# Kernel tuning notes

Hardware: AMD Instinct MI355X
Metric: run time of the kernel (lower is better)

Reference implementation:

```python
import jax, jax.numpy as jnp
import numpy as np

N_NODES = 50000
N_EDGES = 800000
IN_CH = 64
HID = 64
N_LAYERS = 4


def setup_inputs() -> dict:
    key = jax.random.key(0)
    ks = jax.random.split(key, 10)
    x = jax.random.normal(ks[0], (N_NODES, IN_CH), dtype=jnp.float32)
    edge_index = jax.random.randint(ks[1], (2, N_EDGES), 0, N_NODES, dtype=jnp.int32)
    # SAGEConv params per layer: lin_l (applied to aggregated neighbors, with bias)
    # and lin_r (applied to root node). All layers are 64->64 so stack to [L, in, out].
    s = 1.0 / np.sqrt(IN_CH)
    Wl = jax.random.uniform(ks[2], (N_LAYERS, IN_CH, HID), jnp.float32, -s, s)
    Wr = jax.random.uniform(ks[3], (N_LAYERS, IN_CH, HID), jnp.float32, -s, s)
    b = jax.random.uniform(ks[4], (N_LAYERS, HID), jnp.float32, -s, s)
    alpha = jnp.full((N_LAYERS, HID), 0.25, dtype=jnp.float32)  # PReLU init
    return {"x": x, "edge_index": edge_index, "Wl": Wl, "Wr": Wr, "b": b, "alpha": alpha}


def _sage_layer(x, src, dst, deg_inv, Wl, Wr, b):
    # mean aggregation of source-node features at destination nodes
    agg = jax.ops.segment_sum(x[src], dst, num_segments=N_NODES)  # [N, d]
    agg = agg * deg_inv[:, None]
    return agg @ Wl + x @ Wr + b


def _prelu(x, a):
    return jnp.where(x >= 0, x, a * x)


def reference(x, edge_index, Wl, Wr, b, alpha):
    src, dst = edge_index[0], edge_index[1]
    deg = jax.ops.segment_sum(jnp.ones((N_EDGES,), jnp.float32), dst, num_segments=N_NODES)
    deg_inv = 1.0 / jnp.maximum(deg, 1.0)
    for i in range(N_LAYERS):
        x = _sage_layer(x, src, dst, deg_inv, Wl[i], Wr[i], b[i])
        x = _prelu(x, alpha[i])
    return x
```

## Files before the change

kernel.cpp:

```cpp
#include <hip/hip_runtime.h>

#define NN 50000
#define NE 800000
#define C 64
#define NL 4
#define SCAN_NB 196

typedef __attribute__((ext_vector_type(8))) short bf16x8;
typedef __attribute__((ext_vector_type(4))) float f32x4;

__device__ __forceinline__ unsigned short f2bf(float f) {
    unsigned u = __float_as_uint(f);
    u += 0x7fffu + ((u >> 16) & 1u);
    return (unsigned short)(u >> 16);
}
__device__ __forceinline__ float4 bf4_to_f4(uint2 p) {
    float4 r;
    r.x = __uint_as_float(p.x << 16);
    r.y = __uint_as_float(p.x & 0xffff0000u);
    r.z = __uint_as_float(p.y << 16);
    r.w = __uint_as_float(p.y & 0xffff0000u);
    return r;
}

__global__ void init_kernel(int4* __restrict__ p) {
    int i = blockIdx.x * blockDim.x + threadIdx.x;
    if (i < (NN + 16) / 4) p[i] = make_int4(0, 0, 0, 0);
}

__global__ void hist_rank_kernel(const int* __restrict__ dst, int* __restrict__ deg_cnt,
                                 int* __restrict__ rank) {
    int e = blockIdx.x * blockDim.x + threadIdx.x;
    if (e < NE) rank[e] = atomicAdd(&deg_cnt[dst[e]], 1);
}

__global__ __launch_bounds__(256) void scan1_kernel(const int* __restrict__ deg_cnt,
                                                    int* __restrict__ row_start,
                                                    int* __restrict__ bsums) {
    __shared__ int sdata[256];
    int tid = threadIdx.x;
    int i = blockIdx.x * 256 + tid;
    int v = (i < NN) ? deg_cnt[i] : 0;
    sdata[tid] = v;
    __syncthreads();
    for (int off = 1; off < 256; off <<= 1) {
        int t = (tid >= off) ? sdata[tid - off] : 0;
        __syncthreads();
        sdata[tid] += t;
        __syncthreads();
    }
    int incl = sdata[tid];
    if (i < NN) row_start[i] = incl - v;
    if (tid == 255) bsums[blockIdx.x] = incl;
}

__global__ __launch_bounds__(256) void scan23_kernel(int* __restrict__ row_start,
                                                     const int* __restrict__ bsums,
                                                     const int* __restrict__ deg_cnt,
                                                     float* __restrict__ deg_inv) {
    __shared__ int sdata[256];
    int tid = threadIdx.x;
    int v = (tid < SCAN_NB) ? bsums[tid] : 0;
    sdata[tid] = v;
    __syncthreads();
    for (int off = 1; off < 256; off <<= 1) {
        int t = (tid >= off) ? sdata[tid - off] : 0;
        __syncthreads();
        sdata[tid] += t;
        __syncthreads();
    }
    int b = blockIdx.x;
    int offset = (b == 0) ? 0 : sdata[b - 1];
    int i = b * 256 + tid;
    if (i < NN) {
        row_start[i] += offset;
        deg_inv[i] = 1.0f / fmaxf((float)deg_cnt[i], 1.0f);
    }
}

__global__ void fill_kernel(const int* __restrict__ src, const int* __restrict__ dst,
                            const int* __restrict__ rank, const int* __restrict__ row_start,
                            int* __restrict__ csr_src) {
    int t = blockIdx.x * blockDim.x + threadIdx.x;
    int e0 = t * 4;
    if (e0 + 3 < NE) {
        int4 d4 = ((const int4*)dst)[t];
        int4 r4 = ((const int4*)rank)[t];
        int4 s4 = ((const int4*)src)[t];
        csr_src[row_start[d4.x] + r4.x] = s4.x;
        csr_src[row_start[d4.y] + r4.y] = s4.y;
        csr_src[row_start[d4.z] + r4.z] = s4.z;
        csr_src[row_start[d4.w] + r4.w] = s4.w;
    } else if (e0 < NE) {
        for (int e = e0; e < NE; e++)
            csr_src[row_start[dst[e]] + rank[e]] = src[e];
    }
}

__global__ __launch_bounds__(512) void transform_mfma_kernel(
    const float* __restrict__ xin,
    const float* __restrict__ Wl, const float* __restrict__ Wr,
    const float* __restrict__ bias,
    unsigned short* __restrict__ y, float* __restrict__ z)
{
    __shared__ unsigned short xs[64][72];
    __shared__ unsigned short wlT[64][72];
    __shared__ unsigned short wrT[64][72];
    __shared__ unsigned short ys[64][64];
    __shared__ float zs[64][64];
    __shared__ float bs[C];

    int tid = threadIdx.x;
    int node0 = blockIdx.x * 64;

    for (int i = tid; i < C * C; i += 512) {
        int k = i >> 6, c = i & 63;
        wlT[c][k] = f2bf(Wl[i]);
        wrT[c][k] = f2bf(Wr[i]);
    }
    if (tid < C) bs[tid] = bias[tid];
    for (int i = tid; i < 64 * 16; i += 512) {
        int nl = i >> 4, c4 = i & 15;
        int n = node0 + nl;
        int nc = n < NN ? n : NN - 1;
        float4 v = ((const float4*)xin)[(size_t)nc * 16 + c4];
        xs[nl][c4 * 4 + 0] = f2bf(v.x);
        xs[nl][c4 * 4 + 1] = f2bf(v.y);
        xs[nl][c4 * 4 + 2] = f2bf(v.z);
        xs[nl][c4 * 4 + 3] = f2bf(v.w);
    }
    __syncthreads();

    int w = tid >> 6;
    int l = tid & 63;
    int mt = w >> 1;
    int half = w & 1;
    int r16 = l & 15;
    int kg = l >> 4;

    bf16x8 a0 = *(const bf16x8*)&xs[mt * 16 + r16][kg * 8];
    bf16x8 a1 = *(const bf16x8*)&xs[mt * 16 + r16][32 + kg * 8];

    f32x4 acc[4];
    #pragma unroll
    for (int nt = 0; nt < 4; nt++) {
        float bv = half ? bs[nt * 16 + r16] : 0.f;
        acc[nt] = (f32x4){bv, bv, bv, bv};
    }
    #pragma unroll
    for (int nt = 0; nt < 4; nt++) {
        const unsigned short* col = half ? &wrT[nt * 16 + r16][0] : &wlT[nt * 16 + r16][0];
        bf16x8 b0 = *(const bf16x8*)&col[kg * 8];
        bf16x8 b1 = *(const bf16x8*)&col[32 + kg * 8];
        acc[nt] = __builtin_amdgcn_mfma_f32_16x16x32_bf16(a0, b0, acc[nt], 0, 0, 0);
        acc[nt] = __builtin_amdgcn_mfma_f32_16x16x32_bf16(a1, b1, acc[nt], 0, 0, 0);
    }
    #pragma unroll
    for (int nt = 0; nt < 4; nt++) {
        #pragma unroll
        for (int j = 0; j < 4; j++) {
            int r = mt * 16 + kg * 4 + j;
            int c = nt * 16 + r16;
            if (half) zs[r][c] = acc[nt][j];
            else      ys[r][c] = f2bf(acc[nt][j]);
        }
    }
    __syncthreads();

    for (int i = tid; i < 64 * 16; i += 512) {
        int r = i >> 4, g = i & 15;
        int n = node0 + r;
        if (n < NN) {
            ((ushort4*)&y[(size_t)n * C])[g] = ((const ushort4*)&ys[r][0])[g];
            ((float4*)&z[(size_t)n * C])[g] = ((const float4*)&zs[r][0])[g];
        }
    }
}

__device__ __forceinline__ float4 gather_row(const uint2* __restrict__ yb,
                                             const int* __restrict__ cp, int d, int ql) {
    float4 acc = make_float4(0.f, 0.f, 0.f, 0.f);
    for (int t = 0; t < d; t += 8) {
        int lim = d - 1 - t;
        int j1 = min(1, lim), j2 = min(2, lim), j3 = min(3, lim);
        int j4 = min(4, lim), j5 = min(5, lim), j6 = min(6, lim), j7 = min(7, lim);
        float m1 = lim >= 1 ? 1.f : 0.f, m2 = lim >= 2 ? 1.f : 0.f;
        float m3 = lim >= 3 ? 1.f : 0.f, m4 = lim >= 4 ? 1.f : 0.f;
        float m5 = lim >= 5 ? 1.f : 0.f, m6 = lim >= 6 ? 1.f : 0.f;
        float m7 = lim >= 7 ? 1.f : 0.f;
        int s0 = cp[t];
        int s1 = cp[t + j1];
        int s2 = cp[t + j2];
        int s3 = cp[t + j3];
        int s4 = cp[t + j4];
        int s5 = cp[t + j5];
        int s6 = cp[t + j6];
        int s7 = cp[t + j7];
        uint2 p0 = yb[(size_t)s0 * 16 + ql];
        uint2 p1 = yb[(size_t)s1 * 16 + ql];
        uint2 p2 = yb[(size_t)s2 * 16 + ql];
        uint2 p3 = yb[(size_t)s3 * 16 + ql];
        uint2 p4 = yb[(size_t)s4 * 16 + ql];
        uint2 p5 = yb[(size_t)s5 * 16 + ql];
        uint2 p6 = yb[(size_t)s6 * 16 + ql];
        uint2 p7 = yb[(size_t)s7 * 16 + ql];
        float4 v0 = bf4_to_f4(p0);
        float4 v1 = bf4_to_f4(p1);
        float4 v2 = bf4_to_f4(p2);
        float4 v3 = bf4_to_f4(p3);
        float4 v4 = bf4_to_f4(p4);
        float4 v5 = bf4_to_f4(p5);
        float4 v6 = bf4_to_f4(p6);
        float4 v7 = bf4_to_f4(p7);
        acc.x += v0.x;      acc.y += v0.y;      acc.z += v0.z;      acc.w += v0.w;
        acc.x += v1.x * m1; acc.y += v1.y * m1; acc.z += v1.z * m1; acc.w += v1.w * m1;
        acc.x += v2.x * m2; acc.y += v2.y * m2; acc.z += v2.z * m2; acc.w += v2.w * m2;
        acc.x += v3.x * m3; acc.y += v3.y * m3; acc.z += v3.z * m3; acc.w += v3.w * m3;
        acc.x += v4.x * m4; acc.y += v4.y * m4; acc.z += v4.z * m4; acc.w += v4.w * m4;
        acc.x += v5.x * m5; acc.y += v5.y * m5; acc.z += v5.z * m5; acc.w += v5.w * m5;
        acc.x += v6.x * m6; acc.y += v6.y * m6; acc.z += v6.z * m6; acc.w += v6.w * m6;
        acc.x += v7.x * m7; acc.y += v7.y * m7; acc.z += v7.z * m7; acc.w += v7.w * m7;
    }
    return acc;
}

__global__ __launch_bounds__(512) void fused_gt_kernel(
    const uint2* __restrict__ yb, const float4* __restrict__ z4,
    const int* __restrict__ row_start, const int* __restrict__ deg_cnt,
    const float* __restrict__ deg_inv, const float* __restrict__ alpha,
    const int* __restrict__ csr_src,
    const float* __restrict__ Wl2, const float* __restrict__ Wr2,
    const float* __restrict__ bias2,
    unsigned short* __restrict__ yout, float* __restrict__ zout)
{
    __shared__ unsigned short wlT[64][72];
    __shared__ unsigned short wrT[64][72];
    __shared__ unsigned short xsb[32][72];
    __shared__ unsigned short ys[32][64];
    __shared__ float zs[32][64];
    __shared__ float bs2[C];

    int tid = threadIdx.x;
    for (int i = tid; i < C * C; i += 512) {
        int k = i >> 6, c = i & 63;
        wlT[c][k] = f2bf(Wl2[i]);
        wrT[c][k] = f2bf(Wr2[i]);
    }
    if (tid < C) bs2[tid] = bias2[tid];

    int nl = tid >> 4;
    int ql = tid & 15;
    int n = blockIdx.x * 32 + nl;

    float4 o = make_float4(0.f, 0.f, 0.f, 0.f);
    if (n < NN) {
        int rs = row_start[n];
        int d = deg_cnt[n];
        float4 acc = gather_row(yb, csr_src + rs, d, ql);
        float di = deg_inv[n];
        float4 zz = z4[(size_t)n * 16 + ql];
        float4 a4 = ((const float4*)alpha)[ql];
        o.x = di * acc.x + zz.x;
        o.y = di * acc.y + zz.y;
        o.z = di * acc.z + zz.z;
        o.w = di * acc.w + zz.w;
        o.x = o.x >= 0.f ? o.x : a4.x * o.x;
        o.y = o.y >= 0.f ? o.y : a4.y * o.y;
        o.z = o.z >= 0.f ? o.z : a4.z * o.z;
        o.w = o.w >= 0.f ? o.w : a4.w * o.w;
    }
    {
        ushort4 p = make_ushort4(f2bf(o.x), f2bf(o.y), f2bf(o.z), f2bf(o.w));
        *(ushort4*)&xsb[nl][ql * 4] = p;
    }
    __syncthreads();

    int w = tid >> 6;
    int l = tid & 63;
    int mt = w & 1;
    int half = (w >> 1) & 1;
    int ntg = w >> 2;
    int r16 = l & 15;
    int kg = l >> 4;

    bf16x8 a0 = *(const bf16x8*)&xsb[mt * 16 + r16][kg * 8];
    bf16x8 a1 = *(const bf16x8*)&xsb[mt * 16 + r16][32 + kg * 8];

    #pragma unroll
    for (int q = 0; q < 2; q++) {
        int nt = ntg * 2 + q;
        const unsigned short* col = half ? &wrT[nt * 16 + r16][0] : &wlT[nt * 16 + r16][0];
        bf16x8 b0 = *(const bf16x8*)&col[kg * 8];
        bf16x8 b1 = *(const bf16x8*)&col[32 + kg * 8];
        float bv = half ? bs2[nt * 16 + r16] : 0.f;
        f32x4 acc = (f32x4){bv, bv, bv, bv};
        acc = __builtin_amdgcn_mfma_f32_16x16x32_bf16(a0, b0, acc, 0, 0, 0);
        acc = __builtin_amdgcn_mfma_f32_16x16x32_bf16(a1, b1, acc, 0, 0, 0);
        #pragma unroll
        for (int j = 0; j < 4; j++) {
            int r = mt * 16 + kg * 4 + j;
            int c = nt * 16 + r16;
            if (half) zs[r][c] = acc[j];
            else      ys[r][c] = f2bf(acc[j]);
        }
    }
    __syncthreads();

    {
        int r = tid >> 4, g = tid & 15;
        int n2 = blockIdx.x * 32 + r;
        if (n2 < NN) {
            ((ushort4*)&yout[(size_t)n2 * C])[g] = ((const ushort4*)&ys[r][0])[g];
            ((float4*)&zout[(size_t)n2 * C])[g] = ((const float4*)&zs[r][0])[g];
        }
    }
}

__global__ __launch_bounds__(256) void gather_kernel(
    const uint2* __restrict__ yb, const float4* __restrict__ z4,
    const int* __restrict__ row_start, const int* __restrict__ deg_cnt,
    const float* __restrict__ deg_inv, const float* __restrict__ alpha,
    const int* __restrict__ csr_src,
    float4* __restrict__ out4)
{
    int tid = threadIdx.x;
    int n = blockIdx.x * 16 + (tid >> 4);
    int ql = tid & 15;

    int rs = row_start[n];
    int d = deg_cnt[n];
    float4 acc = gather_row(yb, csr_src + rs, d, ql);

    float di = deg_inv[n];
    float4 zz = z4[(size_t)n * 16 + ql];
    float4 a4 = ((const float4*)alpha)[ql];
    float4 o;
    o.x = di * acc.x + zz.x;
    o.y = di * acc.y + zz.y;
    o.z = di * acc.z + zz.z;
    o.w = di * acc.w + zz.w;
    o.x = o.x >= 0.f ? o.x : a4.x * o.x;
    o.y = o.y >= 0.f ? o.y : a4.y * o.y;
    o.z = o.z >= 0.f ? o.z : a4.z * o.z;
    o.w = o.w >= 0.f ? o.w : a4.w * o.w;
    out4[(size_t)n * 16 + ql] = o;
}

extern "C" void kernel_launch(void* const* d_in, const int* in_sizes, int n_in,
                              void* d_out, int out_size, void* d_ws, size_t ws_size,
                              hipStream_t stream) {
    const float* x     = (const float*)d_in[0];
    const int*   ei    = (const int*)d_in[1];
    const float* Wl    = (const float*)d_in[2];
    const float* Wr    = (const float*)d_in[3];
    const float* b     = (const float*)d_in[4];
    const float* alpha = (const float*)d_in[5];
    float* out = (float*)d_out;

    const int* src = ei;
    const int* dst = ei + NE;

    char* wsp = (char*)d_ws;
    int*   deg_cnt   = (int*)wsp;                   wsp += (size_t)(NN + 16) * 4;
    float* deg_inv   = (float*)wsp;                 wsp += (size_t)NN * 4;
    int*   row_start = (int*)wsp;                   wsp += (size_t)NN * 4;
    int*   bsums     = (int*)wsp;                   wsp += 1024;
    int*   rankb     = (int*)wsp;                   wsp += (size_t)NE * 4;
    int*   csr_src   = (int*)wsp;                   wsp += (size_t)NE * 4;
    unsigned short* y0buf = (unsigned short*)wsp;   wsp += (size_t)NN * C * 2;
    unsigned short* y1buf = (unsigned short*)wsp;   wsp += (size_t)NN * C * 2;
    float* z0buf     = (float*)wsp;                 wsp += (size_t)NN * C * 4;
    float* z1buf     = (float*)wsp;

    init_kernel<<<49, 256, 0, stream>>>((int4*)deg_cnt);
    hist_rank_kernel<<<(NE + 255) / 256, 256, 0, stream>>>(dst, deg_cnt, rankb);
    scan1_kernel<<<SCAN_NB, 256, 0, stream>>>(deg_cnt, row_start, bsums);
    scan23_kernel<<<SCAN_NB, 256, 0, stream>>>(row_start, bsums, deg_cnt, deg_inv);
    fill_kernel<<<(NE / 4 + 255) / 256, 256, 0, stream>>>(src, dst, rankb, row_start, csr_src);

    transform_mfma_kernel<<<(NN + 63) / 64, 512, 0, stream>>>(x, Wl, Wr, b, y0buf, z0buf);

    const int fblocks = (NN + 31) / 32;
    unsigned short* ycur = y0buf; float* zcur = z0buf;
    unsigned short* ynxt = y1buf; float* znxt = z1buf;
    for (int l = 0; l < NL - 1; l++) {
        fused_gt_kernel<<<fblocks, 512, 0, stream>>>(
            (const uint2*)ycur, (const float4*)zcur,
            row_start, deg_cnt, deg_inv, alpha + (size_t)l * C, csr_src,
            Wl + (size_t)(l + 1) * C * C, Wr + (size_t)(l + 1) * C * C,
            b + (size_t)(l + 1) * C,
            ynxt, znxt);
        unsigned short* ty = ycur; float* tz = zcur;
        ycur = ynxt; zcur = znxt;
        ynxt = ty;   znxt = tz;
    }

    gather_kernel<<<NN / 16, 256, 0, stream>>>(
        (const uint2*)ycur, (const float4*)zcur, row_start, deg_cnt,
        deg_inv, alpha + (size_t)(NL - 1) * C, csr_src, (float4*)out);
}
```

Measured before the change: 172.2 us.

## Build CSR via two-level bucket sort with shared-memory atomics

Replaces the global-atomic histogram, rank and scatter CSR build with a two-level counting sort. Edges are first bucketed by dst>>8 using per-block shared-memory counters and a per-bucket prefix scan. Each 256-node bucket then computes degrees and fills CSR with local shared atomics. This avoids contended global atomics and random global scatter, at the cost of more kernel launches and an extra pass over an int2 sorted edge array. Within-node neighbor order becomes nondeterministic, but the sum is order-independent up to rounding.

```diff
diff --git a/kernel.cpp b/kernel.cpp
--- a/kernel.cpp
+++ b/kernel.cpp
@@ -5,6 +5,8 @@
 #define C 64
 #define NL 4
 #define SCAN_NB 196
+#define NBK 196
+#define HBLK 782
 
 typedef __attribute__((ext_vector_type(8))) short bf16x8;
 typedef __attribute__((ext_vector_type(4))) float f32x4;
@@ -23,24 +25,91 @@
     return r;
 }
 
-__global__ void init_kernel(int4* __restrict__ p) {
-    int i = blockIdx.x * blockDim.x + threadIdx.x;
-    if (i < (NN + 16) / 4) p[i] = make_int4(0, 0, 0, 0);
-}
-
-__global__ void hist_rank_kernel(const int* __restrict__ dst, int* __restrict__ deg_cnt,
-                                 int* __restrict__ rank) {
-    int e = blockIdx.x * blockDim.x + threadIdx.x;
-    if (e < NE) rank[e] = atomicAdd(&deg_cnt[dst[e]], 1);
-}
-
-__global__ __launch_bounds__(256) void scan1_kernel(const int* __restrict__ deg_cnt,
+__global__ __launch_bounds__(1024) void bucket_hist_kernel(const int* __restrict__ dst,
+                                                           int* __restrict__ blk_cnt,
+                                                           int* __restrict__ lrank) {
+    __shared__ int cnt[NBK];
+    int tid = threadIdx.x;
+    int blk = blockIdx.x;
+    if (tid < NBK) cnt[tid] = 0;
+    __syncthreads();
+    int e = blk * 1024 + tid;
+    if (e < NE) lrank[e] = atomicAdd(&cnt[dst[e] >> 8], 1);
+    __syncthreads();
+    if (tid < NBK) blk_cnt[tid * HBLK + blk] = cnt[tid];
+}
+
+__global__ __launch_bounds__(1024) void scanblk_kernel(int* __restrict__ blk_cnt,
+                                                       int* __restrict__ bucket_tot) {
+    __shared__ int sdata[1024];
+    int b = blockIdx.x;
+    int tid = threadIdx.x;
+    int v = (tid < HBLK) ? blk_cnt[b * HBLK + tid] : 0;
+    sdata[tid] = v;
+    __syncthreads();
+    for (int off = 1; off < 1024; off <<= 1) {
+        int t = (tid >= off) ? sdata[tid - off] : 0;
+        __syncthreads();
+        sdata[tid] += t;
+        __syncthreads();
+    }
+    if (tid < HBLK) blk_cnt[b * HBLK + tid] = sdata[tid] - v;
+    if (tid == HBLK - 1) bucket_tot[b] = sdata[tid];
+}
+
+__global__ __launch_bounds__(256) void scanbucket_kernel(const int* __restrict__ bucket_tot,
+                                                         int* __restrict__ bucket_start) {
+    __shared__ int sdata[256];
+    int tid = threadIdx.x;
+    int v = (tid < NBK) ? bucket_tot[tid] : 0;
+    sdata[tid] = v;
+    __syncthreads();
+    for (int off = 1; off < 256; off <<= 1) {
+        int t = (tid >= off) ? sdata[tid - off] : 0;
+        __syncthreads();
+        sdata[tid] += t;
+        __syncthreads();
+    }
+    if (tid < NBK) bucket_start[tid] = sdata[tid] - v;
+    if (tid == NBK - 1) bucket_start[NBK] = sdata[tid];
+}
+
+__global__ __launch_bounds__(1024) void bucket_scatter_kernel(
+    const int* __restrict__ src, const int* __restrict__ dst,
+    const int* __restrict__ lrank, const int* __restrict__ base2,
+    const int* __restrict__ bucket_start, int2* __restrict__ sorted) {
+    int blk = blockIdx.x;
+    int e = blk * 1024 + threadIdx.x;
+    if (e < NE) {
+        int d = dst[e];
+        int b = d >> 8;
+        int pos = bucket_start[b] + base2[b * HBLK + blk] + lrank[e];
+        sorted[pos] = make_int2(src[e], d);
+    }
+}
+
+__global__ __launch_bounds__(512) void bucket_deg_kernel(const int2* __restrict__ sorted,
+                                                         const int* __restrict__ bucket_start,
+                                                         int* __restrict__ deg) {
+    __shared__ int ldeg[256];
+    int b = blockIdx.x;
+    int tid = threadIdx.x;
+    if (tid < 256) ldeg[tid] = 0;
+    __syncthreads();
+    int lo = bucket_start[b], hi = bucket_start[b + 1];
+    for (int i = lo + tid; i < hi; i += 512)
+        atomicAdd(&ldeg[sorted[i].y & 255], 1);
+    __syncthreads();
+    if (tid < 256) deg[b * 256 + tid] = ldeg[tid];
+}
+
+__global__ __launch_bounds__(256) void scan1_kernel(const int* __restrict__ deg,
                                                     int* __restrict__ row_start,
                                                     int* __restrict__ bsums) {
     __shared__ int sdata[256];
     int tid = threadIdx.x;
     int i = blockIdx.x * 256 + tid;
-    int v = (i < NN) ? deg_cnt[i] : 0;
+    int v = (i < NN) ? deg[i] : 0;
     sdata[tid] = v;
     __syncthreads();
     for (int off = 1; off < 256; off <<= 1) {
@@ -56,7 +125,7 @@
 
 __global__ __launch_bounds__(256) void scan23_kernel(int* __restrict__ row_start,
                                                      const int* __restrict__ bsums,
-                                                     const int* __restrict__ deg_cnt,
+                                                     const int* __restrict__ deg,
                                                      float* __restrict__ deg_inv) {
     __shared__ int sdata[256];
     int tid = threadIdx.x;
@@ -74,26 +143,29 @@
     int i = b * 256 + tid;
     if (i < NN) {
         row_start[i] += offset;
-        deg_inv[i] = 1.0f / fmaxf((float)deg_cnt[i], 1.0f);
-    }
-}
-
-__global__ void fill_kernel(const int* __restrict__ src, const int* __restrict__ dst,
-                            const int* __restrict__ rank, const int* __restrict__ row_start,
-                            int* __restrict__ csr_src) {
-    int t = blockIdx.x * blockDim.x + threadIdx.x;
-    int e0 = t * 4;
-    if (e0 + 3 < NE) {
-        int4 d4 = ((const int4*)dst)[t];
-        int4 r4 = ((const int4*)rank)[t];
-        int4 s4 = ((const int4*)src)[t];
-        csr_src[row_start[d4.x] + r4.x] = s4.x;
-        csr_src[row_start[d4.y] + r4.y] = s4.y;
-        csr_src[row_start[d4.z] + r4.z] = s4.z;
-        csr_src[row_start[d4.w] + r4.w] = s4.w;
-    } else if (e0 < NE) {
-        for (int e = e0; e < NE; e++)
-            csr_src[row_start[dst[e]] + rank[e]] = src[e];
+        deg_inv[i] = 1.0f / fmaxf((float)deg[i], 1.0f);
+    }
+}
+
+__global__ __launch_bounds__(512) void bucket_fill_kernel(const int2* __restrict__ sorted,
+                                                          const int* __restrict__ bucket_start,
+                                                          const int* __restrict__ row_start,
+                                                          int* __restrict__ csr_src) {
+    __shared__ int rs[256];
+    __shared__ int lcnt[256];
+    int b = blockIdx.x;
+    int tid = threadIdx.x;
+    if (tid < 256) {
+        int n = b * 256 + tid;
+        rs[tid] = (n < NN) ? row_start[n] : 0;
+        lcnt[tid] = 0;
+    }
+    __syncthreads();
+    int lo = bucket_start[b], hi = bucket_start[b + 1];
+    for (int i = lo + tid; i < hi; i += 512) {
+        int2 p = sorted[i];
+        int r = atomicAdd(&lcnt[p.y & 255], 1);
+        csr_src[rs[p.y & 255] + r] = p.x;
     }
 }
 
@@ -226,7 +298,7 @@
 
 __global__ __launch_bounds__(512) void fused_gt_kernel(
     const uint2* __restrict__ yb, const float4* __restrict__ z4,
-    const int* __restrict__ row_start, const int* __restrict__ deg_cnt,
+    const int* __restrict__ row_start, const int* __restrict__ deg,
     const float* __restrict__ deg_inv, const float* __restrict__ alpha,
     const int* __restrict__ csr_src,
     const float* __restrict__ Wl2, const float* __restrict__ Wr2,
@@ -255,7 +327,7 @@
     float4 o = make_float4(0.f, 0.f, 0.f, 0.f);
     if (n < NN) {
         int rs = row_start[n];
-        int d = deg_cnt[n];
+        int d = deg[n];
         float4 acc = gather_row(yb, csr_src + rs, d, ql);
         float di = deg_inv[n];
         float4 zz = z4[(size_t)n * 16 + ql];
@@ -318,7 +390,7 @@
 
 __global__ __launch_bounds__(256) void gather_kernel(
     const uint2* __restrict__ yb, const float4* __restrict__ z4,
-    const int* __restrict__ row_start, const int* __restrict__ deg_cnt,
+    const int* __restrict__ row_start, const int* __restrict__ deg,
     const float* __restrict__ deg_inv, const float* __restrict__ alpha,
     const int* __restrict__ csr_src,
     float4* __restrict__ out4)
@@ -328,7 +400,7 @@
     int ql = tid & 15;
 
     int rs = row_start[n];
-    int d = deg_cnt[n];
+    int d = deg[n];
     float4 acc = gather_row(yb, csr_src + rs, d, ql);
 
     float di = deg_inv[n];
@@ -361,22 +433,30 @@
     const int* dst = ei + NE;
 
     char* wsp = (char*)d_ws;
-    int*   deg_cnt   = (int*)wsp;                   wsp += (size_t)(NN + 16) * 4;
-    float* deg_inv   = (float*)wsp;                 wsp += (size_t)NN * 4;
-    int*   row_start = (int*)wsp;                   wsp += (size_t)NN * 4;
-    int*   bsums     = (int*)wsp;                   wsp += 1024;
-    int*   rankb     = (int*)wsp;                   wsp += (size_t)NE * 4;
-    int*   csr_src   = (int*)wsp;                   wsp += (size_t)NE * 4;
+    int*  lrank        = (int*)wsp;                 wsp += (size_t)NE * 4;
+    int*  blk_cnt      = (int*)wsp;                 wsp += (size_t)NBK * HBLK * 4 + 256;
+    int*  bucket_tot   = (int*)wsp;                 wsp += 1024;
+    int*  bucket_start = (int*)wsp;                 wsp += 1024;
+    int2* sorted       = (int2*)wsp;                wsp += (size_t)NE * 8;
+    int*  deg          = (int*)wsp;                 wsp += (size_t)(NBK * 256) * 4;
+    float* deg_inv     = (float*)wsp;               wsp += (size_t)NN * 4;
+    int*  row_start    = (int*)wsp;                 wsp += (size_t)NN * 4;
+    int*  bsums        = (int*)wsp;                 wsp += 1024;
     unsigned short* y0buf = (unsigned short*)wsp;   wsp += (size_t)NN * C * 2;
     unsigned short* y1buf = (unsigned short*)wsp;   wsp += (size_t)NN * C * 2;
-    float* z0buf     = (float*)wsp;                 wsp += (size_t)NN * C * 4;
-    float* z1buf     = (float*)wsp;
-
-    init_kernel<<<49, 256, 0, stream>>>((int4*)deg_cnt);
-    hist_rank_kernel<<<(NE + 255) / 256, 256, 0, stream>>>(dst, deg_cnt, rankb);
-    scan1_kernel<<<SCAN_NB, 256, 0, stream>>>(deg_cnt, row_start, bsums);
-    scan23_kernel<<<SCAN_NB, 256, 0, stream>>>(row_start, bsums, deg_cnt, deg_inv);
-    fill_kernel<<<(NE / 4 + 255) / 256, 256, 0, stream>>>(src, dst, rankb, row_start, csr_src);
+    float* z0buf       = (float*)wsp;               wsp += (size_t)NN * C * 4;
+    float* z1buf       = (float*)wsp;
+    int*  csr_src      = lrank;
+
+    bucket_hist_kernel<<<HBLK, 1024, 0, stream>>>(dst, blk_cnt, lrank);
+    scanblk_kernel<<<NBK, 1024, 0, stream>>>(blk_cnt, bucket_tot);
+    scanbucket_kernel<<<1, 256, 0, stream>>>(bucket_tot, bucket_start);
+    bucket_scatter_kernel<<<HBLK, 1024, 0, stream>>>(src, dst, lrank, blk_cnt,
+                                                     bucket_start, sorted);
+    bucket_deg_kernel<<<NBK, 512, 0, stream>>>(sorted, bucket_start, deg);
+    scan1_kernel<<<SCAN_NB, 256, 0, stream>>>(deg, row_start, bsums);
+    scan23_kernel<<<SCAN_NB, 256, 0, stream>>>(row_start, bsums, deg, deg_inv);
+    bucket_fill_kernel<<<NBK, 512, 0, stream>>>(sorted, bucket_start, row_start, csr_src);
 
     transform_mfma_kernel<<<(NN + 63) / 64, 512, 0, stream>>>(x, Wl, Wr, b, y0buf, z0buf);
 
@@ -386,7 +466,7 @@
     for (int l = 0; l < NL - 1; l++) {
         fused_gt_kernel<<<fblocks, 512, 0, stream>>>(
             (const uint2*)ycur, (const float4*)zcur,
-            row_start, deg_cnt, deg_inv, alpha + (size_t)l * C, csr_src,
+            row_start, deg, deg_inv, alpha + (size_t)l * C, csr_src,
             Wl + (size_t)(l + 1) * C * C, Wr + (size_t)(l + 1) * C * C,
             b + (size_t)(l + 1) * C,
             ynxt, znxt);
@@ -396,6 +476,6 @@
     }
 
     gather_kernel<<<NN / 16, 256, 0, stream>>>(
-        (const uint2*)ycur, (const float4*)zcur, row_start, deg_cnt,
+        (const uint2*)ycur, (const float4*)zcur, row_start, deg,
         deg_inv, alpha + (size_t)(NL - 1) * C, csr_src, (float4*)out);
 }
```

Result: faster. 163.9 us (-4.8%).
